# Kernel optimization log

Measured on AMD Instinct MI355X. Metric: run time of the kernel, lower is better.

## Reference

```python
import jax, jax.numpy as jnp
import numpy as np

B, C, L, O = 32, 256, 336, 96
K, NLAYERS, DFF = 4, 2, 1024
EPS = 1e-5


def setup_inputs() -> dict:
    key = jax.random.key(0)
    ks = jax.random.split(key, 10)
    s1 = 1.0 / np.sqrt(L)
    s2 = 1.0 / np.sqrt(DFF)
    return {
        "x": jax.random.normal(ks[0], (B, C, L), dtype=jnp.float32),
        "rev_w": jnp.ones((C,), dtype=jnp.float32),
        "rev_b": jnp.zeros((C,), dtype=jnp.float32),
        "W1": jax.random.normal(ks[1], (K, NLAYERS, L, DFF), dtype=jnp.float32) * s1,
        "b1": jnp.zeros((K, NLAYERS, DFF), dtype=jnp.float32),
        "W2": jax.random.normal(ks[2], (K, NLAYERS, DFF, L), dtype=jnp.float32) * s2,
        "b2": jnp.zeros((K, NLAYERS, L), dtype=jnp.float32),
        "Wh": jax.random.normal(ks[3], (K, L, O), dtype=jnp.float32) * s1,
        "bh": jnp.zeros((K, O), dtype=jnp.float32),
        "assign": jax.random.randint(ks[4], (C,), 0, K, dtype=jnp.int32),
    }


def reference(x, rev_w, rev_b, W1, b1, W2, b2, Wh, bh, assign):
    # RevIN norm over the time axis, per instance and per channel. x: [B,C,L]
    mean = jnp.mean(x, axis=-1, keepdims=True)
    std = jnp.sqrt(jnp.var(x, axis=-1, keepdims=True) + EPS)
    xn = (x - mean) / std * rev_w[None, :, None] + rev_b[None, :, None]

    n_clusters = Wh.shape[0]
    n_layers = W1.shape[1]
    out = jnp.zeros(x.shape[:2] + (Wh.shape[-1],), dtype=x.dtype)  # [B,C,O]
    for k in range(n_clusters):
        z = xn  # [B,C,L] time-mixing MLP stack shared across channels
        for l in range(n_layers):
            h = jax.nn.relu(jnp.einsum('bcl,ld->bcd', z, W1[k, l]) + b1[k, l])
            z = z + jnp.einsum('bcd,dl->bcl', h, W2[k, l]) + b2[k, l]
        y = jnp.einsum('bcl,lo->bco', z, Wh[k]) + bh[k]  # [B,C,O]
        out = jnp.where((assign == k)[None, :, None], y, out)

    # RevIN denorm, then transpose to [B, out_len, C]
    out = (out - rev_b[None, :, None]) / rev_w[None, :, None] * std + mean
    return jnp.transpose(out, (0, 2, 1))
```

## Files before the change

kernel.cpp:

```cpp
#include <hip/hip_runtime.h>
#include <math.h>


typedef unsigned short u16;
typedef unsigned int u32;
typedef unsigned long long u64;

constexpr int B = 32, C = 256, L = 336, O = 96, K = 4, NL = 2, DFF = 1024;
constexpr int TM = 32;
constexpr int NTILES = (B * C) / TM;
constexpr int LP = 352;
constexpr int KS1 = LP / 32;
constexpr int KS2 = DFF / 32;
constexpr int NT2 = LP / 16;
constexpr int NTH = O / 16;
constexpr int ZBS = 360;
constexpr int HS = 1032;

constexpr int W1FRAGS = (DFF / 16) * KS1 * 64;
constexpr int W2FRAGS = NT2 * KS2 * 64;
constexpr int WHFRAGS = NTH * KS1 * 64;
constexpr int NW1 = W1FRAGS * K * NL;
constexpr int NW2 = W2FRAGS * K * NL;
constexpr int NPREP = 176 + 256 + 44 + 1;

typedef __bf16 bf16x8 __attribute__((ext_vector_type(8)));
typedef float f32x4 __attribute__((ext_vector_type(4)));

__device__ __forceinline__ u16 f2bf(float f) {
  union { float f; u32 u; } v;
  v.f = f;
  u32 r = v.u + 0x7fffu + ((v.u >> 16) & 1u);
  return (u16)(r >> 16);
}
__device__ __forceinline__ float bf2f(u16 h) {
  union { u32 u; float f; } v;
  v.u = ((u32)h) << 16;
  return v.f;
}
__device__ __forceinline__ u32 pack2(float a, float b) {
  return (u32)f2bf(a) | ((u32)f2bf(b) << 16);
}

__global__ __launch_bounds__(256) void prep(const int* __restrict__ assign,
                                            const float* __restrict__ W1,
                                            const float* __restrict__ W2,
                                            const float* __restrict__ Wh,
                                            int* __restrict__ meta,
                                            u16* __restrict__ wbuf) {
  __shared__ u16 sm[32][516];
  const int bid = blockIdx.x;
  const int tid = threadIdx.x;
  const int wid = tid >> 6, lane = tid & 63;
  const int q = lane >> 4, rm = lane & 15;

  if (bid < 176) {
    const int dh = bid & 1;
    const int ks = (bid >> 1) % 11;
    const int kl = bid / 22;
    for (int rr = 0; rr < 8; ++rr) {
      const int r = wid * 8 + rr;
      const int l = ks * 32 + r;
#pragma unroll
      for (int h = 0; h < 2; ++h) {
        const int c = h * 256 + lane * 4;
        float4 v = make_float4(0.f, 0.f, 0.f, 0.f);
        if (l < L)
          v = *(const float4*)(W1 + ((size_t)kl * L + l) * DFF + dh * 512 + c);
        uint2 p;
        p.x = pack2(v.x, v.y);
        p.y = pack2(v.z, v.w);
        *(uint2*)&sm[r][c] = p;
      }
    }
    __syncthreads();
    for (int e = 0; e < 8; ++e) {
      const int ntl = wid * 8 + e;
      const int nt = dh * 32 + ntl;
      u32 w4[4];
#pragma unroll
      for (int jj = 0; jj < 4; ++jj) {
        const u16 a = sm[q * 8 + 2 * jj][ntl * 16 + rm];
        const u16 b = sm[q * 8 + 2 * jj + 1][ntl * 16 + rm];
        w4[jj] = (u32)a | ((u32)b << 16);
      }
      uint4 o;
      o.x = w4[0]; o.y = w4[1]; o.z = w4[2]; o.w = w4[3];
      *(uint4*)(wbuf + ((size_t)(kl * 64 + nt) * 11 + ks) * 512 + lane * 8) = o;
    }
  } else if (bid < 432) {
    const int b2i = bid - 176;
    const int ks = b2i & 31;
    const int kl = b2i >> 5;
    for (int rr = 0; rr < 8; ++rr) {
      const int r = wid * 8 + rr;
      const float* row = W2 + ((size_t)kl * DFF + ks * 32 + r) * L;
      {
        const int c = lane * 4;
        const float4 v = *(const float4*)(row + c);
        uint2 p;
        p.x = pack2(v.x, v.y);
        p.y = pack2(v.z, v.w);
        *(uint2*)&sm[r][c] = p;
      }
      {
        const int c = 256 + lane * 4;
        if (c < 352) {
          float4 v = make_float4(0.f, 0.f, 0.f, 0.f);
          if (c < L) v = *(const float4*)(row + c);
          uint2 p;
          p.x = pack2(v.x, v.y);
          p.y = pack2(v.z, v.w);
          *(uint2*)&sm[r][c] = p;
        }
      }
    }
    __syncthreads();
    for (int nt = wid; nt < NT2; nt += 4) {
      u32 w4[4];
#pragma unroll
      for (int jj = 0; jj < 4; ++jj) {
        const u16 a = sm[q * 8 + 2 * jj][nt * 16 + rm];
        const u16 b = sm[q * 8 + 2 * jj + 1][nt * 16 + rm];
        w4[jj] = (u32)a | ((u32)b << 16);
      }
      uint4 o;
      o.x = w4[0]; o.y = w4[1]; o.z = w4[2]; o.w = w4[3];
      *(uint4*)(wbuf + (size_t)NW1 * 8 +
                ((size_t)(kl * 22 + nt) * 32 + ks) * 512 + lane * 8) = o;
    }
  } else if (bid < 476) {
    const int b3i = bid - 432;
    const int ks = b3i % 11;
    const int kk = b3i / 11;
    for (int rr = 0; rr < 8; ++rr) {
      const int r = wid * 8 + rr;
      const int l = ks * 32 + r;
      if (lane < 24) {
        const int c = lane * 4;
        float4 v = make_float4(0.f, 0.f, 0.f, 0.f);
        if (l < L) v = *(const float4*)(Wh + ((size_t)kk * L + l) * O + c);
        uint2 p;
        p.x = pack2(v.x, v.y);
        p.y = pack2(v.z, v.w);
        *(uint2*)&sm[r][c] = p;
      }
    }
    __syncthreads();
    for (int nt = wid; nt < NTH; nt += 4) {
      u32 w4[4];
#pragma unroll
      for (int jj = 0; jj < 4; ++jj) {
        const u16 a = sm[q * 8 + 2 * jj][nt * 16 + rm];
        const u16 b = sm[q * 8 + 2 * jj + 1][nt * 16 + rm];
        w4[jj] = (u32)a | ((u32)b << 16);
      }
      uint4 o;
      o.x = w4[0]; o.y = w4[1]; o.z = w4[2]; o.w = w4[3];
      *(uint4*)(wbuf + (size_t)(NW1 + NW2) * 8 +
                ((size_t)(kk * 6 + nt) * 11 + ks) * 512 + lane * 8) = o;
    }
  } else {
    __shared__ int wcnt[4][K];
    __shared__ int pre[4][K];
    __shared__ int cofs[K + 1];
    const int a = assign[tid];
    const u64 below = (1ull << lane) - 1ull;
    int myrank = 0;
#pragma unroll
    for (int k = 0; k < K; ++k) {
      const u64 m = __ballot(a == k);
      if (a == k) myrank = (int)__popcll(m & below);
      if (lane == 0) wcnt[wid][k] = (int)__popcll(m);
    }
    __syncthreads();
    if (tid == 0) {
      int tot[K];
      for (int k = 0; k < K; ++k) {
        int s = 0;
        for (int ww = 0; ww < 4; ++ww) {
          pre[ww][k] = s;
          s += wcnt[ww][k];
        }
        tot[k] = s;
      }
      cofs[0] = 0;
      for (int k = 0; k < K; ++k) cofs[k + 1] = cofs[k] + tot[k];
      for (int k = 0; k <= K; ++k) meta[512 + k] = cofs[k];
    }
    __syncthreads();
    const int pos = cofs[a] + pre[wid][a] + myrank;
    meta[256 + pos] = tid;
    int k = 0;
    while (k < K - 1 && tid >= cofs[k + 1]) ++k;
    meta[tid] = (k << 16) | ((tid - cofs[k]) * TM);
  }
}

__global__ __launch_bounds__(1024, 4) void mlp_mfma(
    const float* __restrict__ x, const float* __restrict__ rev_w,
    const float* __restrict__ rev_b, const float* __restrict__ b1,
    const float* __restrict__ b2, const float* __restrict__ bh,
    const int* __restrict__ meta, const u16* __restrict__ wbuf,
    float* __restrict__ out) {
  __shared__ __align__(16) u16 zb[TM][ZBS];
  __shared__ __align__(16) u16 Hsh[TM][HS];
  __shared__ float s_mean[TM], s_std[TM], s_rw[TM], s_rb[TM];
  __shared__ int s_b[TM], s_c[TM];

  const int tid = threadIdx.x;
  const int wid = tid >> 6;
  const int lane = tid & 63;
  const int q = lane >> 4, rm = lane & 15;

  const int swz = (blockIdx.x & 7) * 32 + (blockIdx.x >> 3);
  const int info = meta[swz];
  const int kcl = info >> 16;
  const int rstart = info & 0xffff;
  const int cofs = meta[512 + kcl];
  const int cnt = meta[512 + kcl + 1] - cofs;

  for (int i = 0; i < 2; ++i) {
    const int t = wid * 2 + i;
    const int ri = rstart + t;
    const int b = ri / cnt;
    const int c = meta[256 + cofs + (ri % cnt)];
    const float* xrow = x + (size_t)(b * C + c) * L;
    float v[6], s = 0.f, s2 = 0.f;
#pragma unroll
    for (int jj = 0; jj < 6; ++jj) {
      const int j = lane + jj * 64;
      v[jj] = (j < L) ? xrow[j] : 0.f;
      s += v[jj];
      s2 += v[jj] * v[jj];
    }
#pragma unroll
    for (int off = 32; off > 0; off >>= 1) {
      s += __shfl_down(s, off);
      s2 += __shfl_down(s2, off);
    }
    s = __shfl(s, 0);
    s2 = __shfl(s2, 0);
    const float mean = s * (1.f / L);
    const float var = s2 * (1.f / L) - mean * mean;
    const float stdv = sqrtf(var + 1e-5f);
    const float rstd = 1.f / stdv;
    const float rw = rev_w[c], rb_ = rev_b[c];
#pragma unroll
    for (int jj = 0; jj < 6; ++jj) {
      const int j = lane + jj * 64;
      if (j < L) zb[t][j] = f2bf((v[jj] - mean) * rstd * rw + rb_);
    }
    if (lane < LP - L) zb[t][L + lane] = 0;
    if (lane == 0) {
      s_mean[t] = mean;
      s_std[t] = stdv;
      s_rw[t] = rw;
      s_rb[t] = rb_;
      s_b[t] = b;
      s_c[t] = c;
    }
  }

  const u16* w1b = wbuf;
  const u16* w2b = wbuf + (size_t)NW1 * 8;
  const u16* whb = wbuf + (size_t)(NW1 + NW2) * 8;
  constexpr int TS1 = KS1 * 512;
  constexpr int TS2 = KS2 * 512;

  bf16x8 acur[4], anxt[4];
  {
    const u16* base = w1b + (size_t)(kcl * NL) * W1FRAGS * 8 +
                      (size_t)(wid * 4) * TS1 + lane * 8;
#pragma unroll
    for (int t = 0; t < 4; ++t) {
      acur[t] = *(const bf16x8*)(base + (size_t)t * TS1);
      anxt[t] = *(const bf16x8*)(base + (size_t)t * TS1 + 512);
    }
  }
  __syncthreads();

  f32x4 zm[2][2];
#pragma unroll
  for (int tt = 0; tt < 2; ++tt) {
    const int nt2 = wid + 16 * tt;
#pragma unroll
    for (int rg = 0; rg < 2; ++rg) {
      if (nt2 < NT2) {
        const uint2 zw = *(const uint2*)&zb[rm + 16 * rg][nt2 * 16 + q * 4];
        zm[tt][rg] = f32x4{bf2f((u16)zw.x), bf2f((u16)(zw.x >> 16)),
                           bf2f((u16)zw.y), bf2f((u16)(zw.y >> 16))};
      } else {
        zm[tt][rg] = f32x4{0.f, 0.f, 0.f, 0.f};
      }
    }
  }

  for (int l = 0; l < NL; ++l) {
    const int kl = kcl * NL + l;
    const u16* W1f = w1b + (size_t)kl * W1FRAGS * 8;
    const u16* W2f = w2b + (size_t)kl * W2FRAGS * 8;
    const float* b1p = b1 + kl * DFF;
    const float* b2p = b2 + kl * L;
    const u16* base1 = W1f + (size_t)(wid * 4) * TS1 + lane * 8;

    f32x4 acc[4][2];
#pragma unroll
    for (int t = 0; t < 4; ++t)
#pragma unroll
      for (int rg = 0; rg < 2; ++rg) acc[t][rg] = f32x4{0.f, 0.f, 0.f, 0.f};
#pragma unroll 2
    for (int ks = 0; ks < KS1; ++ks) {
      bf16x8 ause[4];
#pragma unroll
      for (int t = 0; t < 4; ++t) {
        ause[t] = acur[t];
        acur[t] = anxt[t];
      }
      if (ks + 2 < KS1) {
#pragma unroll
        for (int t = 0; t < 4; ++t)
          anxt[t] = *(const bf16x8*)(base1 + (size_t)t * TS1 + (ks + 2) * 512);
      }
      const bf16x8 zf0 = *(const bf16x8*)&zb[rm][ks * 32 + q * 8];
      const bf16x8 zf1 = *(const bf16x8*)&zb[rm + 16][ks * 32 + q * 8];
#pragma unroll
      for (int t = 0; t < 4; ++t) {
        acc[t][0] = __builtin_amdgcn_mfma_f32_16x16x32_bf16(ause[t], zf0,
                                                            acc[t][0], 0, 0, 0);
        acc[t][1] = __builtin_amdgcn_mfma_f32_16x16x32_bf16(ause[t], zf1,
                                                            acc[t][1], 0, 0, 0);
      }
    }
#pragma unroll
    for (int t = 0; t < 4; ++t) {
      const int nt = wid * 4 + t;
      const float4 bq = *(const float4*)(b1p + nt * 16 + q * 4);
#pragma unroll
      for (int rg = 0; rg < 2; ++rg) {
        uint2 hw;
        hw.x = pack2(fmaxf(acc[t][rg][0] + bq.x, 0.f),
                     fmaxf(acc[t][rg][1] + bq.y, 0.f));
        hw.y = pack2(fmaxf(acc[t][rg][2] + bq.z, 0.f),
                     fmaxf(acc[t][rg][3] + bq.w, 0.f));
        *(uint2*)&Hsh[rm + 16 * rg][nt * 16 + q * 4] = hw;
      }
    }

    const u16* base2 = W2f + lane * 8;
    bf16x8 wq0[2], wq1[2], wq2[2];
#pragma unroll
    for (int tt = 0; tt < 2; ++tt) {
      const int nt2 = wid + 16 * tt;
      if (nt2 < NT2) {
        wq0[tt] = *(const bf16x8*)(base2 + (size_t)nt2 * TS2);
        wq1[tt] = *(const bf16x8*)(base2 + (size_t)nt2 * TS2 + 512);
        wq2[tt] = *(const bf16x8*)(base2 + (size_t)nt2 * TS2 + 1024);
      }
    }
    __syncthreads();

#pragma unroll 2
    for (int ks = 0; ks < KS2; ++ks) {
      bf16x8 wuse[2];
#pragma unroll
      for (int tt = 0; tt < 2; ++tt) {
        wuse[tt] = wq0[tt];
        wq0[tt] = wq1[tt];
        wq1[tt] = wq2[tt];
      }
      if (ks + 3 < KS2) {
#pragma unroll
        for (int tt = 0; tt < 2; ++tt) {
          const int nt2 = wid + 16 * tt;
          if (nt2 < NT2)
            wq2[tt] =
                *(const bf16x8*)(base2 + (size_t)nt2 * TS2 + (ks + 3) * 512);
        }
      }
      const bf16x8 hf0 = *(const bf16x8*)&Hsh[rm][ks * 32 + q * 8];
      const bf16x8 hf1 = *(const bf16x8*)&Hsh[rm + 16][ks * 32 + q * 8];
#pragma unroll
      for (int tt = 0; tt < 2; ++tt) {
        if (wid + 16 * tt < NT2) {
          zm[tt][0] = __builtin_amdgcn_mfma_f32_16x16x32_bf16(wuse[tt], hf0,
                                                              zm[tt][0], 0, 0, 0);
          zm[tt][1] = __builtin_amdgcn_mfma_f32_16x16x32_bf16(wuse[tt], hf1,
                                                              zm[tt][1], 0, 0, 0);
        }
      }
    }

#pragma unroll
    for (int tt = 0; tt < 2; ++tt) {
      const int nt2 = wid + 16 * tt;
      if (nt2 < NT2) {
        const int lc = nt2 * 16 + q * 4;
        if (lc < L) {
          const float4 bq = *(const float4*)(b2p + lc);
          zm[tt][0][0] += bq.x; zm[tt][0][1] += bq.y;
          zm[tt][0][2] += bq.z; zm[tt][0][3] += bq.w;
          zm[tt][1][0] += bq.x; zm[tt][1][1] += bq.y;
          zm[tt][1][2] += bq.z; zm[tt][1][3] += bq.w;
        }
#pragma unroll
        for (int rg = 0; rg < 2; ++rg) {
          uint2 zw;
          zw.x = pack2(zm[tt][rg][0], zm[tt][rg][1]);
          zw.y = pack2(zm[tt][rg][2], zm[tt][rg][3]);
          *(uint2*)&zb[rm + 16 * rg][lc] = zw;
        }
      }
    }

    if (l + 1 < NL) {
      const u16* nb = w1b + (size_t)(kl + 1) * W1FRAGS * 8 +
                      (size_t)(wid * 4) * TS1 + lane * 8;
#pragma unroll
      for (int t = 0; t < 4; ++t) {
        acur[t] = *(const bf16x8*)(nb + (size_t)t * TS1);
        anxt[t] = *(const bf16x8*)(nb + (size_t)t * TS1 + 512);
      }
    }
    __syncthreads();
  }

  if (wid < NTH) {
    const u16* Whf =
        whb + (size_t)kcl * WHFRAGS * 8 + (size_t)wid * TS1 + lane * 8;
    f32x4 acc0 = {0.f, 0.f, 0.f, 0.f}, acc1 = {0.f, 0.f, 0.f, 0.f};
    for (int ks = 0; ks < KS1; ++ks) {
      const bf16x8 af = *(const bf16x8*)(Whf + ks * 512);
      const bf16x8 zf0 = *(const bf16x8*)&zb[rm][ks * 32 + q * 8];
      const bf16x8 zf1 = *(const bf16x8*)&zb[rm + 16][ks * 32 + q * 8];
      acc0 = __builtin_amdgcn_mfma_f32_16x16x32_bf16(af, zf0, acc0, 0, 0, 0);
      acc1 = __builtin_amdgcn_mfma_f32_16x16x32_bf16(af, zf1, acc1, 0, 0, 0);
    }
    const float4 bq = *(const float4*)(bh + kcl * O + wid * 16 + q * 4);
    const float bqa[4] = {bq.x, bq.y, bq.z, bq.w};
#pragma unroll
    for (int rg = 0; rg < 2; ++rg) {
      const int row = rm + 16 * rg;
      const float mean = s_mean[row], stdv = s_std[row];
      const float rw = s_rw[row], rb_ = s_rb[row];
      const int ob = s_b[row], oc = s_c[row];
      const f32x4 acc = rg ? acc1 : acc0;
#pragma unroll
      for (int gg = 0; gg < 4; ++gg) {
        const int o = wid * 16 + q * 4 + gg;
        const float y = acc[gg] + bqa[gg];
        out[((size_t)ob * O + o) * C + oc] = (y - rb_) / rw * stdv + mean;
      }
    }
  }
}

extern "C" void kernel_launch(void* const* d_in, const int* in_sizes, int n_in,
                              void* d_out, int out_size, void* d_ws,
                              size_t ws_size, hipStream_t stream) {
  const float* x = (const float*)d_in[0];
  const float* rev_w = (const float*)d_in[1];
  const float* rev_b = (const float*)d_in[2];
  const float* W1 = (const float*)d_in[3];
  const float* b1 = (const float*)d_in[4];
  const float* W2 = (const float*)d_in[5];
  const float* b2 = (const float*)d_in[6];
  const float* Wh = (const float*)d_in[7];
  const float* bh = (const float*)d_in[8];
  const int* assign = (const int*)d_in[9];
  float* out = (float*)d_out;

  int* meta = (int*)d_ws;
  u16* wbuf = (u16*)((char*)d_ws + 4096);

  prep<<<NPREP, 256, 0, stream>>>(assign, W1, W2, Wh, meta, wbuf);
  mlp_mfma<<<NTILES, 1024, 0, stream>>>(x, rev_w, rev_b, b1, b2, bh, meta,
                                        wbuf, out);
}
```

Before: 168.6 us.

## Switch MLP GEMMs to 32x32x16 MFMA with re-laid-out weight fragments

Repacks the W1 and W2 bf16 fragments in the prep kernel for the 32x32x16 MFMA shape and rewrites both MLP GEMMs in the main kernel to use it. Each wave now covers a 32-row by 32-column output tile with one f32x16 accumulator, which halves the number of MFMA issues and the LDS operand reads per FLOP. Weight prefetching becomes a deeper ring buffer (4 slots for W1, 8 for W2) with fully unrolled loops. In exchange, the W2 stage runs on only 11 of 16 waves instead of 16, and register pressure goes up under the 1024-thread launch bound.

```diff
diff --git a/kernel.cpp b/kernel.cpp
--- a/kernel.cpp
+++ b/kernel.cpp
@@ -10,22 +10,30 @@
 constexpr int TM = 32;
 constexpr int NTILES = (B * C) / TM;
 constexpr int LP = 352;
-constexpr int KS1 = LP / 32;
-constexpr int KS2 = DFF / 32;
-constexpr int NT2 = LP / 16;
-constexpr int NTH = O / 16;
 constexpr int ZBS = 360;
 constexpr int HS = 1032;
 
-constexpr int W1FRAGS = (DFF / 16) * KS1 * 64;
-constexpr int W2FRAGS = NT2 * KS2 * 64;
-constexpr int WHFRAGS = NTH * KS1 * 64;
+constexpr int DT1 = 32;
+constexpr int KT1 = 22;
+constexpr int LT2 = 11;
+constexpr int KT2 = 64;
+constexpr int NTH = 6;
+constexpr int KSH = 11;
+
+constexpr int TS1 = KT1 * 512;
+constexpr int TS2 = KT2 * 512;
+constexpr int THS = KSH * 512;
+
+constexpr int W1FRAGS = DT1 * KT1 * 64;
+constexpr int W2FRAGS = LT2 * KT2 * 64;
+constexpr int WHFRAGS = NTH * KSH * 64;
 constexpr int NW1 = W1FRAGS * K * NL;
 constexpr int NW2 = W2FRAGS * K * NL;
 constexpr int NPREP = 176 + 256 + 44 + 1;
 
 typedef __bf16 bf16x8 __attribute__((ext_vector_type(8)));
 typedef float f32x4 __attribute__((ext_vector_type(4)));
+typedef float f32x16 __attribute__((ext_vector_type(16)));
 
 __device__ __forceinline__ u16 f2bf(float f) {
   union { float f; u32 u; } v;
@@ -53,14 +61,15 @@
   const int tid = threadIdx.x;
   const int wid = tid >> 6, lane = tid & 63;
   const int q = lane >> 4, rm = lane & 15;
+  const int q2 = lane >> 5, n32 = lane & 31;
 
   if (bid < 176) {
     const int dh = bid & 1;
-    const int ks = (bid >> 1) % 11;
+    const int ks32 = (bid >> 1) % 11;
     const int kl = bid / 22;
     for (int rr = 0; rr < 8; ++rr) {
       const int r = wid * 8 + rr;
-      const int l = ks * 32 + r;
+      const int l = ks32 * 32 + r;
 #pragma unroll
       for (int h = 0; h < 2; ++h) {
         const int c = h * 256 + lane * 4;
@@ -75,26 +84,27 @@
     }
     __syncthreads();
     for (int e = 0; e < 8; ++e) {
-      const int ntl = wid * 8 + e;
-      const int nt = dh * 32 + ntl;
+      const int item = wid * 8 + e;
+      const int dtl = item >> 1, half = item & 1;
+      const int rb = 16 * half + q2 * 8;
+      const int col = dtl * 32 + n32;
+      uint4 o;
       u32 w4[4];
 #pragma unroll
-      for (int jj = 0; jj < 4; ++jj) {
-        const u16 a = sm[q * 8 + 2 * jj][ntl * 16 + rm];
-        const u16 b = sm[q * 8 + 2 * jj + 1][ntl * 16 + rm];
-        w4[jj] = (u32)a | ((u32)b << 16);
-      }
-      uint4 o;
+      for (int jj = 0; jj < 4; ++jj)
+        w4[jj] = (u32)sm[rb + 2 * jj][col] | ((u32)sm[rb + 2 * jj + 1][col] << 16);
       o.x = w4[0]; o.y = w4[1]; o.z = w4[2]; o.w = w4[3];
-      *(uint4*)(wbuf + ((size_t)(kl * 64 + nt) * 11 + ks) * 512 + lane * 8) = o;
+      const int dt = dh * 16 + dtl;
+      const int ks = ks32 * 2 + half;
+      *(uint4*)(wbuf + ((size_t)(kl * DT1 + dt) * KT1 + ks) * 512 + lane * 8) = o;
     }
   } else if (bid < 432) {
     const int b2i = bid - 176;
-    const int ks = b2i & 31;
+    const int ks32 = b2i & 31;
     const int kl = b2i >> 5;
     for (int rr = 0; rr < 8; ++rr) {
       const int r = wid * 8 + rr;
-      const float* row = W2 + ((size_t)kl * DFF + ks * 32 + r) * L;
+      const float* row = W2 + ((size_t)kl * DFF + ks32 * 32 + r) * L;
       {
         const int c = lane * 4;
         const float4 v = *(const float4*)(row + c);
@@ -116,18 +126,19 @@
       }
     }
     __syncthreads();
-    for (int nt = wid; nt < NT2; nt += 4) {
+    for (int item = wid; item < 22; item += 4) {
+      const int lt = item >> 1, half = item & 1;
+      const int rb = 16 * half + q2 * 8;
+      const int col = 32 * lt + n32;
+      uint4 o;
       u32 w4[4];
 #pragma unroll
-      for (int jj = 0; jj < 4; ++jj) {
-        const u16 a = sm[q * 8 + 2 * jj][nt * 16 + rm];
-        const u16 b = sm[q * 8 + 2 * jj + 1][nt * 16 + rm];
-        w4[jj] = (u32)a | ((u32)b << 16);
-      }
-      uint4 o;
+      for (int jj = 0; jj < 4; ++jj)
+        w4[jj] = (u32)sm[rb + 2 * jj][col] | ((u32)sm[rb + 2 * jj + 1][col] << 16);
       o.x = w4[0]; o.y = w4[1]; o.z = w4[2]; o.w = w4[3];
+      const int ks = ks32 * 2 + half;
       *(uint4*)(wbuf + (size_t)NW1 * 8 +
-                ((size_t)(kl * 22 + nt) * 32 + ks) * 512 + lane * 8) = o;
+                ((size_t)(kl * LT2 + lt) * KT2 + ks) * 512 + lane * 8) = o;
     }
   } else if (bid < 476) {
     const int b3i = bid - 432;
@@ -148,6 +159,7 @@
     }
     __syncthreads();
     for (int nt = wid; nt < NTH; nt += 4) {
+      uint4 o;
       u32 w4[4];
 #pragma unroll
       for (int jj = 0; jj < 4; ++jj) {
@@ -155,10 +167,9 @@
         const u16 b = sm[q * 8 + 2 * jj + 1][nt * 16 + rm];
         w4[jj] = (u32)a | ((u32)b << 16);
       }
-      uint4 o;
       o.x = w4[0]; o.y = w4[1]; o.z = w4[2]; o.w = w4[3];
       *(uint4*)(wbuf + (size_t)(NW1 + NW2) * 8 +
-                ((size_t)(kk * 6 + nt) * 11 + ks) * 512 + lane * 8) = o;
+                ((size_t)(kk * NTH + nt) * KSH + ks) * 512 + lane * 8) = o;
     }
   } else {
     __shared__ int wcnt[4][K];
@@ -212,6 +223,7 @@
   const int wid = tid >> 6;
   const int lane = tid & 63;
   const int q = lane >> 4, rm = lane & 15;
+  const int q2 = lane >> 5, n32 = lane & 31;
 
   const int swz = (blockIdx.x & 7) * 32 + (blockIdx.x >> 3);
   const int info = meta[swz];
@@ -265,34 +277,30 @@
   const u16* w1b = wbuf;
   const u16* w2b = wbuf + (size_t)NW1 * 8;
   const u16* whb = wbuf + (size_t)(NW1 + NW2) * 8;
-  constexpr int TS1 = KS1 * 512;
-  constexpr int TS2 = KS2 * 512;
-
-  bf16x8 acur[4], anxt[4];
+
+  bf16x8 a1[2][4];
   {
-    const u16* base = w1b + (size_t)(kcl * NL) * W1FRAGS * 8 +
-                      (size_t)(wid * 4) * TS1 + lane * 8;
-#pragma unroll
-    for (int t = 0; t < 4; ++t) {
-      acur[t] = *(const bf16x8*)(base + (size_t)t * TS1);
-      anxt[t] = *(const bf16x8*)(base + (size_t)t * TS1 + 512);
-    }
+    const u16* b0 = w1b + (size_t)(kcl * NL) * W1FRAGS * 8 +
+                    (size_t)(wid * 2) * TS1 + lane * 8;
+#pragma unroll
+    for (int t = 0; t < 2; ++t)
+#pragma unroll
+      for (int s = 0; s < 4; ++s)
+        a1[t][s] = *(const bf16x8*)(b0 + (size_t)t * TS1 + s * 512);
   }
   __syncthreads();
 
-  f32x4 zm[2][2];
-#pragma unroll
-  for (int tt = 0; tt < 2; ++tt) {
-    const int nt2 = wid + 16 * tt;
-#pragma unroll
-    for (int rg = 0; rg < 2; ++rg) {
-      if (nt2 < NT2) {
-        const uint2 zw = *(const uint2*)&zb[rm + 16 * rg][nt2 * 16 + q * 4];
-        zm[tt][rg] = f32x4{bf2f((u16)zw.x), bf2f((u16)(zw.x >> 16)),
-                           bf2f((u16)zw.y), bf2f((u16)(zw.y >> 16))};
-      } else {
-        zm[tt][rg] = f32x4{0.f, 0.f, 0.f, 0.f};
-      }
+  f32x16 zm;
+#pragma unroll
+  for (int i = 0; i < 16; ++i) zm[i] = 0.f;
+  if (wid < LT2) {
+#pragma unroll
+    for (int g = 0; g < 4; ++g) {
+      const uint2 zw = *(const uint2*)&zb[n32][32 * wid + 8 * g + 4 * q2];
+      zm[4 * g + 0] = bf2f((u16)zw.x);
+      zm[4 * g + 1] = bf2f((u16)(zw.x >> 16));
+      zm[4 * g + 2] = bf2f((u16)zw.y);
+      zm[4 * g + 3] = bf2f((u16)(zw.y >> 16));
     }
   }
 
@@ -302,134 +310,94 @@
     const u16* W2f = w2b + (size_t)kl * W2FRAGS * 8;
     const float* b1p = b1 + kl * DFF;
     const float* b2p = b2 + kl * L;
-    const u16* base1 = W1f + (size_t)(wid * 4) * TS1 + lane * 8;
-
-    f32x4 acc[4][2];
-#pragma unroll
-    for (int t = 0; t < 4; ++t)
-#pragma unroll
-      for (int rg = 0; rg < 2; ++rg) acc[t][rg] = f32x4{0.f, 0.f, 0.f, 0.f};
-#pragma unroll 2
-    for (int ks = 0; ks < KS1; ++ks) {
-      bf16x8 ause[4];
-#pragma unroll
-      for (int t = 0; t < 4; ++t) {
-        ause[t] = acur[t];
-        acur[t] = anxt[t];
-      }
-      if (ks + 2 < KS1) {
-#pragma unroll
-        for (int t = 0; t < 4; ++t)
-          anxt[t] = *(const bf16x8*)(base1 + (size_t)t * TS1 + (ks + 2) * 512);
-      }
-      const bf16x8 zf0 = *(const bf16x8*)&zb[rm][ks * 32 + q * 8];
-      const bf16x8 zf1 = *(const bf16x8*)&zb[rm + 16][ks * 32 + q * 8];
-#pragma unroll
-      for (int t = 0; t < 4; ++t) {
-        acc[t][0] = __builtin_amdgcn_mfma_f32_16x16x32_bf16(ause[t], zf0,
-                                                            acc[t][0], 0, 0, 0);
-        acc[t][1] = __builtin_amdgcn_mfma_f32_16x16x32_bf16(ause[t], zf1,
-                                                            acc[t][1], 0, 0, 0);
-      }
-    }
-#pragma unroll
-    for (int t = 0; t < 4; ++t) {
-      const int nt = wid * 4 + t;
-      const float4 bq = *(const float4*)(b1p + nt * 16 + q * 4);
-#pragma unroll
-      for (int rg = 0; rg < 2; ++rg) {
+    const u16* base1 = W1f + (size_t)(wid * 2) * TS1 + lane * 8;
+
+    f32x16 acc[2];
+#pragma unroll
+    for (int t = 0; t < 2; ++t)
+#pragma unroll
+      for (int i = 0; i < 16; ++i) acc[t][i] = 0.f;
+#pragma unroll
+    for (int ks = 0; ks < KT1; ++ks) {
+      const bf16x8 zf = *(const bf16x8*)&zb[n32][ks * 16 + q2 * 8];
+#pragma unroll
+      for (int t = 0; t < 2; ++t)
+        acc[t] = __builtin_amdgcn_mfma_f32_32x32x16_bf16(a1[t][ks & 3], zf,
+                                                         acc[t], 0, 0, 0);
+      if (ks + 4 < KT1) {
+#pragma unroll
+        for (int t = 0; t < 2; ++t)
+          a1[t][ks & 3] =
+              *(const bf16x8*)(base1 + (size_t)t * TS1 + (ks + 4) * 512);
+      }
+    }
+#pragma unroll
+    for (int t = 0; t < 2; ++t) {
+      const int dt = wid * 2 + t;
+#pragma unroll
+      for (int g = 0; g < 4; ++g) {
+        const int db = dt * 32 + 8 * g + 4 * q2;
+        const float4 bq = *(const float4*)(b1p + db);
         uint2 hw;
-        hw.x = pack2(fmaxf(acc[t][rg][0] + bq.x, 0.f),
-                     fmaxf(acc[t][rg][1] + bq.y, 0.f));
-        hw.y = pack2(fmaxf(acc[t][rg][2] + bq.z, 0.f),
-                     fmaxf(acc[t][rg][3] + bq.w, 0.f));
-        *(uint2*)&Hsh[rm + 16 * rg][nt * 16 + q * 4] = hw;
-      }
-    }
-
-    const u16* base2 = W2f + lane * 8;
-    bf16x8 wq0[2], wq1[2], wq2[2];
-#pragma unroll
-    for (int tt = 0; tt < 2; ++tt) {
-      const int nt2 = wid + 16 * tt;
-      if (nt2 < NT2) {
-        wq0[tt] = *(const bf16x8*)(base2 + (size_t)nt2 * TS2);
-        wq1[tt] = *(const bf16x8*)(base2 + (size_t)nt2 * TS2 + 512);
-        wq2[tt] = *(const bf16x8*)(base2 + (size_t)nt2 * TS2 + 1024);
-      }
-    }
-    __syncthreads();
-
-#pragma unroll 2
-    for (int ks = 0; ks < KS2; ++ks) {
-      bf16x8 wuse[2];
-#pragma unroll
-      for (int tt = 0; tt < 2; ++tt) {
-        wuse[tt] = wq0[tt];
-        wq0[tt] = wq1[tt];
-        wq1[tt] = wq2[tt];
-      }
-      if (ks + 3 < KS2) {
-#pragma unroll
-        for (int tt = 0; tt < 2; ++tt) {
-          const int nt2 = wid + 16 * tt;
-          if (nt2 < NT2)
-            wq2[tt] =
-                *(const bf16x8*)(base2 + (size_t)nt2 * TS2 + (ks + 3) * 512);
-        }
-      }
-      const bf16x8 hf0 = *(const bf16x8*)&Hsh[rm][ks * 32 + q * 8];
-      const bf16x8 hf1 = *(const bf16x8*)&Hsh[rm + 16][ks * 32 + q * 8];
-#pragma unroll
-      for (int tt = 0; tt < 2; ++tt) {
-        if (wid + 16 * tt < NT2) {
-          zm[tt][0] = __builtin_amdgcn_mfma_f32_16x16x32_bf16(wuse[tt], hf0,
-                                                              zm[tt][0], 0, 0, 0);
-          zm[tt][1] = __builtin_amdgcn_mfma_f32_16x16x32_bf16(wuse[tt], hf1,
-                                                              zm[tt][1], 0, 0, 0);
-        }
-      }
-    }
-
-#pragma unroll
-    for (int tt = 0; tt < 2; ++tt) {
-      const int nt2 = wid + 16 * tt;
-      if (nt2 < NT2) {
-        const int lc = nt2 * 16 + q * 4;
+        hw.x = pack2(fmaxf(acc[t][4 * g + 0] + bq.x, 0.f),
+                     fmaxf(acc[t][4 * g + 1] + bq.y, 0.f));
+        hw.y = pack2(fmaxf(acc[t][4 * g + 2] + bq.z, 0.f),
+                     fmaxf(acc[t][4 * g + 3] + bq.w, 0.f));
+        *(uint2*)&Hsh[n32][db] = hw;
+      }
+    }
+
+    bf16x8 a2[8];
+    const u16* base2 = W2f + (size_t)wid * TS2 + lane * 8;
+    if (wid < LT2) {
+#pragma unroll
+      for (int s = 0; s < 8; ++s)
+        a2[s] = *(const bf16x8*)(base2 + s * 512);
+    }
+    __syncthreads();
+
+    if (wid < LT2) {
+#pragma unroll
+      for (int ks = 0; ks < KT2; ++ks) {
+        const bf16x8 hf = *(const bf16x8*)&Hsh[n32][ks * 16 + q2 * 8];
+        zm = __builtin_amdgcn_mfma_f32_32x32x16_bf16(a2[ks & 7], hf, zm, 0, 0, 0);
+        if (ks + 8 < KT2)
+          a2[ks & 7] = *(const bf16x8*)(base2 + (ks + 8) * 512);
+      }
+#pragma unroll
+      for (int g = 0; g < 4; ++g) {
+        const int lc = 32 * wid + 8 * g + 4 * q2;
         if (lc < L) {
           const float4 bq = *(const float4*)(b2p + lc);
-          zm[tt][0][0] += bq.x; zm[tt][0][1] += bq.y;
-          zm[tt][0][2] += bq.z; zm[tt][0][3] += bq.w;
-          zm[tt][1][0] += bq.x; zm[tt][1][1] += bq.y;
-          zm[tt][1][2] += bq.z; zm[tt][1][3] += bq.w;
+          zm[4 * g + 0] += bq.x;
+          zm[4 * g + 1] += bq.y;
+          zm[4 * g + 2] += bq.z;
+          zm[4 * g + 3] += bq.w;
         }
-#pragma unroll
-        for (int rg = 0; rg < 2; ++rg) {
-          uint2 zw;
-          zw.x = pack2(zm[tt][rg][0], zm[tt][rg][1]);
-          zw.y = pack2(zm[tt][rg][2], zm[tt][rg][3]);
-          *(uint2*)&zb[rm + 16 * rg][lc] = zw;
-        }
+        uint2 zw;
+        zw.x = pack2(zm[4 * g + 0], zm[4 * g + 1]);
+        zw.y = pack2(zm[4 * g + 2], zm[4 * g + 3]);
+        *(uint2*)&zb[n32][lc] = zw;
       }
     }
 
     if (l + 1 < NL) {
       const u16* nb = w1b + (size_t)(kl + 1) * W1FRAGS * 8 +
-                      (size_t)(wid * 4) * TS1 + lane * 8;
-#pragma unroll
-      for (int t = 0; t < 4; ++t) {
-        acur[t] = *(const bf16x8*)(nb + (size_t)t * TS1);
-        anxt[t] = *(const bf16x8*)(nb + (size_t)t * TS1 + 512);
-      }
+                      (size_t)(wid * 2) * TS1 + lane * 8;
+#pragma unroll
+      for (int t = 0; t < 2; ++t)
+#pragma unroll
+        for (int s = 0; s < 4; ++s)
+          a1[t][s] = *(const bf16x8*)(nb + (size_t)t * TS1 + s * 512);
     }
     __syncthreads();
   }
 
   if (wid < NTH) {
     const u16* Whf =
-        whb + (size_t)kcl * WHFRAGS * 8 + (size_t)wid * TS1 + lane * 8;
+        whb + (size_t)kcl * WHFRAGS * 8 + (size_t)wid * THS + lane * 8;
     f32x4 acc0 = {0.f, 0.f, 0.f, 0.f}, acc1 = {0.f, 0.f, 0.f, 0.f};
-    for (int ks = 0; ks < KS1; ++ks) {
+    for (int ks = 0; ks < KSH; ++ks) {
       const bf16x8 af = *(const bf16x8*)(Whf + ks * 512);
       const bf16x8 zf0 = *(const bf16x8*)&zb[rm][ks * 32 + q * 8];
       const bf16x8 zf1 = *(const bf16x8*)&zb[rm + 16][ks * 32 + q * 8];
```

Result: faster. 143.2 us (-15.0%).
